# Kernel optimization log

Measured on AMD Instinct MI355X. Metric: run time of the kernel, lower is better.

Reference implementation:

```python
import jax, jax.numpy as jnp
import numpy as np

H = 16      # num_heads
G = 4       # num_groups (kv heads)
D = 128     # head_dim = embed_size // num_heads
E = 2048    # embed_size
FF = 8192   # GeGLU hidden = 4 * embed_size
EPS = 1e-6


def setup_inputs() -> dict:
    key = jax.random.key(0)
    ks = jax.random.split(key, 8)
    s = 0.02
    return {
        "x": jax.random.normal(ks[0], (2, 2048, E), dtype=jnp.float32),
        "wq": jax.random.normal(ks[1], (E, H * D), dtype=jnp.float32) * s,
        "wk": jax.random.normal(ks[2], (E, G * D), dtype=jnp.float32) * s,
        "wv": jax.random.normal(ks[3], (E, G * D), dtype=jnp.float32) * s,
        "wo": jax.random.normal(ks[4], (H * D, E), dtype=jnp.float32) * s,
        "norm1_w": jnp.ones((E,), dtype=jnp.float32),
        "norm2_w": jnp.ones((E,), dtype=jnp.float32),
        "w_in": jax.random.normal(ks[5], (E, 2 * FF), dtype=jnp.float32) * s,
        "w_out": jax.random.normal(ks[6], (FF, E), dtype=jnp.float32) * s,
    }


def rotate_half(t):
    t1, t2 = jnp.split(t, 2, axis=-1)
    return jnp.concatenate([-t2, t1], axis=-1)


def rope_cos_sin(n, d, dtype):
    inv_freq = 1.0 / (10000.0 ** (jnp.arange(0, d, 2, dtype=jnp.float32) / d))
    freqs = jnp.outer(jnp.arange(n, dtype=jnp.float32), inv_freq)  # [n, d/2]
    emb = jnp.concatenate([freqs, freqs], axis=-1)                 # [n, d]
    return jnp.cos(emb).astype(dtype), jnp.sin(emb).astype(dtype)


def rmsnorm(t, w):
    return t * jax.lax.rsqrt(jnp.mean(t * t, axis=-1, keepdims=True) + EPS) * w


def reference(x, wq, wk, wv, wo, norm1_w, norm2_w, w_in, w_out):
    b, n, _ = x.shape
    # q = k = v = x.view(b,n,H,D).transpose(1,2); RoPE applied to q,k (v stays raw)
    qh = x.reshape(b, n, H, D).transpose(0, 2, 1, 3)  # [b,H,n,D]
    cos, sin = rope_cos_sin(n, D, x.dtype)
    q_rot = qh * cos + rotate_half(qh) * sin          # q == k pre-RoPE -> same rotation
    k_rot = q_rot
    # flatten back: [b,n,E]; v flattened equals original x (unrotated)
    qf = q_rot.transpose(0, 2, 1, 3).reshape(b, n, E)
    kf = k_rot.transpose(0, 2, 1, 3).reshape(b, n, E)
    vf = x
    # GroupedQueryAttention: q->H heads, k/v->G kv-heads, causal
    qp = (qf @ wq).reshape(b, n, H, D).transpose(0, 2, 1, 3)          # [b,H,n,D]
    kp = (kf @ wk).reshape(b, n, G, D).transpose(0, 2, 1, 3)          # [b,G,n,D]
    vp = (vf @ wv).reshape(b, n, G, D).transpose(0, 2, 1, 3)          # [b,G,n,D]
    rep = H // G
    kp = jnp.repeat(kp, rep, axis=1)                                  # [b,H,n,D]
    vp = jnp.repeat(vp, rep, axis=1)
    scale = 1.0 / jnp.sqrt(jnp.asarray(D, dtype=x.dtype))
    scores = jnp.einsum("bhqd,bhkd->bhqk", qp, kp) * scale
    causal = jnp.tril(jnp.ones((n, n), dtype=bool))
    scores = jnp.where(causal, scores, jnp.asarray(-1e30, dtype=scores.dtype))
    attn = jax.nn.softmax(scores, axis=-1)
    ctx = jnp.einsum("bhqk,bhkd->bhqd", attn, vp)
    attn_out = ctx.transpose(0, 2, 1, 3).reshape(b, n, E) @ wo
    # residual + RMSNorm, GeGLU MLP, residual + RMSNorm
    h = rmsnorm(x + attn_out, norm1_w)
    hg = h @ w_in
    a, g = jnp.split(hg, 2, axis=-1)
    fc = (jax.nn.gelu(a, approximate=False) * g) @ w_out
    out = rmsnorm(h + fc, norm2_w)
    return out
```

## Files before the change

kernel.cpp:

```cpp
#include <hip/hip_runtime.h>
#include <hip/hip_bf16.h>

typedef __bf16 bf16x8 __attribute__((ext_vector_type(8)));
typedef short  s16x8  __attribute__((ext_vector_type(8)));
typedef float  f32x4  __attribute__((ext_vector_type(4)));

__device__ __forceinline__ float bf2f(short u) {
    unsigned x = ((unsigned)(unsigned short)u) << 16;
    float f; __builtin_memcpy(&f, &x, 4); return f;
}
__device__ __forceinline__ short f2bf(float f) {
    unsigned u; __builtin_memcpy(&u, &f, 4);
    unsigned r = (u + 0x7fff + ((u >> 16) & 1)) >> 16;
    return (short)r;
}
__device__ __forceinline__ bool src_is_f32(const void* ones_w) {
    return ((const unsigned short*)ones_w)[0] == 0;
}
__device__ __forceinline__ void gl2lds16(const short* g, short* lds_base) {
    __builtin_amdgcn_global_load_lds((const __attribute__((address_space(1))) void*)g,
                                     (__attribute__((address_space(3))) void*)lds_base, 16, 0, 0);
}
__device__ __forceinline__ bf16x8 lds_read_b128(const short* p) {
    bf16x8 r;
    asm volatile("ds_read_b128 %0, %1"
                 : "=v"(r)
                 : "v"((const __attribute__((address_space(3))) short*)p));
    return r;
}

__global__ __launch_bounds__(256) void rope_kernel(const void* __restrict__ xv, short* __restrict__ qf,
                                                   short* __restrict__ xbf, const void* __restrict__ n1w) {
    bool f32 = src_is_f32(n1w);
    int idx = blockIdx.x * 256 + threadIdx.x;
    int i    = idx & 63;
    int head = (idx >> 6) & 15;
    int t    = idx >> 10;
    int pos  = t & 2047;
    float inv = __expf(-9.210340371976184f * (float)i * (1.0f / 64.0f));
    float fr = (float)pos * inv;
    float s, c; sincosf(fr, &s, &c);
    long base = (long)t * 2048 + head * 128 + i;
    float v1, v2;
    if (f32) { v1 = ((const float*)xv)[base]; v2 = ((const float*)xv)[base + 64]; }
    else     { v1 = bf2f(((const short*)xv)[base]); v2 = bf2f(((const short*)xv)[base + 64]); }
    qf[base]      = f2bf(v1 * c - v2 * s);
    qf[base + 64] = f2bf(v2 * c + v1 * s);
    xbf[base]      = f2bf(v1);
    xbf[base + 64] = f2bf(v2);
}

__global__ __launch_bounds__(256) void transpose_any(const void* __restrict__ src, long soff, long soffz,
                                                     short* __restrict__ dst, long doffz,
                                                     int R, int C, int ld, const void* __restrict__ n1w, int force_bf16) {
    bool f32 = force_bf16 ? false : src_is_f32(n1w);
    __shared__ short tile[32][33];
    int tx = threadIdx.x & 31, ty = threadIdx.x >> 5;
    int c0 = blockIdx.x * 32, r0 = blockIdx.y * 32;
    long sz = soff + soffz * blockIdx.z;
    dst += doffz * blockIdx.z;
    #pragma unroll
    for (int i = 0; i < 32; i += 8) {
        long p = sz + (long)(r0 + ty + i) * ld + c0 + tx;
        tile[ty + i][tx] = f32 ? f2bf(((const float*)src)[p]) : ((const short*)src)[p];
    }
    __syncthreads();
    #pragma unroll
    for (int i = 0; i < 32; i += 8) dst[(long)(c0 + ty + i) * R + r0 + tx] = tile[tx][ty + i];
}

__global__ __launch_bounds__(256) void gemm_nt_kv(const short* __restrict__ A0, const short* __restrict__ A1, int lda,
                                                  const short* __restrict__ Bt0, const short* __restrict__ Bt1,
                                                  short* __restrict__ C0, short* __restrict__ C1, int ldc,
                                                  int M, int N, int K) {
    const short* A  = blockIdx.z ? A1 : A0;
    const short* Bt = blockIdx.z ? Bt1 : Bt0;
    short* C        = blockIdx.z ? C1 : C0;
    __shared__ short As[128 * 64];
    __shared__ short Bs[128 * 64];
    int tid = threadIdx.x;
    int w = tid >> 6, lane = tid & 63, quad = lane >> 4, l15 = lane & 15;
    int m0 = blockIdx.y * 128, n0 = blockIdx.x * 128;
    int wr = (w >> 1) * 64, wc = (w & 1) * 64;
    int srow = (lane >> 3), scol = (lane & 7) * 8;
    f32x4 acc[4][4] = {};
    for (int k0 = 0; k0 < K; k0 += 64) {
        __syncthreads();
        #pragma unroll
        for (int c = 0; c < 4; ++c) {
            int chunk = w * 4 + c;
            int row = chunk * 8 + srow;
            gl2lds16(&A [(long)(m0 + row) * lda + k0 + scol], As + chunk * 512);
            gl2lds16(&Bt[(long)(n0 + row) * K   + k0 + scol], Bs + chunk * 512);
        }
        __syncthreads();
        #pragma unroll
        for (int kk = 0; kk < 64; kk += 32) {
            bf16x8 a[4], b[4];
            #pragma unroll
            for (int i = 0; i < 4; ++i) a[i] = *(const bf16x8*)&As[(wr + 16 * i + l15) * 64 + kk + quad * 8];
            #pragma unroll
            for (int j = 0; j < 4; ++j) b[j] = *(const bf16x8*)&Bs[(wc + 16 * j + l15) * 64 + kk + quad * 8];
            #pragma unroll
            for (int i = 0; i < 4; ++i)
                #pragma unroll
                for (int j = 0; j < 4; ++j)
                    acc[i][j] = __builtin_amdgcn_mfma_f32_16x16x32_bf16(a[i], b[j], acc[i][j], 0, 0, 0);
        }
    }
    #pragma unroll
    for (int i = 0; i < 4; ++i)
        #pragma unroll
        for (int j = 0; j < 4; ++j)
            #pragma unroll
            for (int r = 0; r < 4; ++r)
                C[(long)(m0 + wr + 16 * i + quad * 4 + r) * ldc + n0 + wc + 16 * j + l15] = f2bf(acc[i][j][r]);
}

template<int GEGLU, int ACCUM>
__global__ __launch_bounds__(512) void gemm256(const short* __restrict__ A, int lda,
                                               const short* __restrict__ Bt, const short* __restrict__ Bt2, int ldb,
                                               short* __restrict__ C, short* __restrict__ C2, int ldc,
                                               int M, int N, int K) {
    __shared__ short As[2][256 * 64];
    __shared__ short Bs[2][256 * 64];
    int z = blockIdx.z;
    if (z) { Bt = Bt2; C = C2; }
    A += (long)z * K;
    int tid = threadIdx.x;
    int w = tid >> 6, lane = tid & 63, quad = lane >> 4, l15 = lane & 15;
    int sw = l15 & 7;
    int nbx = gridDim.x, nwg = nbx * gridDim.y;
    int bid = blockIdx.y * nbx + blockIdx.x;
    int swz = (bid & 7) * (nwg >> 3) + (bid >> 3);
    int n0 = (swz % nbx) * 256, m0 = (swz / nbx) * 256;
    int wr2 = (w >> 2) * 128;
    int wcb = (w & 3) * 64;
    int srow = lane >> 3;
    int scol = ((lane & 7) ^ srow) * 8;
    int NT = K >> 6;

    auto STAGE = [&](int bsel, int h, int tt) {
        long kk = (long)((tt < NT) ? tt : 0) * 64;
        int hb = (h & 1) * 8192;
        #pragma unroll
        for (int j = 0; j < 2; ++j) {
            int chunk = j * 8 + w;
            int row = (h & 1) * 128 + chunk * 8 + srow;
            if (h < 2) gl2lds16(&A [(long)(m0 + row) * lda + kk + scol], &As[bsel][hb + chunk * 512]);
            else       gl2lds16(&Bt[(long)(n0 + row) * ldb + kk + scol], &Bs[bsel][hb + chunk * 512]);
        }
    };

    f32x4 acc[8][4] = {};
    STAGE(0, 2, 0); STAGE(0, 3, 0); STAGE(0, 0, 0); STAGE(0, 1, 0);
    STAGE(1, 2, 1); STAGE(1, 3, 1);
    asm volatile("s_waitcnt vmcnt(4)");
    __builtin_amdgcn_s_barrier();

    for (int t = 0; t < NT; ++t) {
        int b = t & 1;
        const short* Ab = As[b];
        const short* Bb = Bs[b];
        bf16x8 bbf[4][2];
        #pragma unroll
        for (int q = 0; q < 4; ++q) {
            if (q == 0) {
                #pragma unroll
                for (int j = 0; j < 4; ++j) {
                    const short* rb = &Bb[(wcb + 16 * j + l15) * 64];
                    bbf[j][0] = lds_read_b128(rb + ((quad ^ sw) * 8));
                    bbf[j][1] = lds_read_b128(rb + (((4 + quad) ^ sw) * 8));
                }
            }
            const short* ra0 = &Ab[(wr2 + 32 * q + l15) * 64];
            const short* ra1 = ra0 + 16 * 64;
            bf16x8 a00 = lds_read_b128(ra0 + ((quad ^ sw) * 8));
            bf16x8 a01 = lds_read_b128(ra0 + (((4 + quad) ^ sw) * 8));
            bf16x8 a10 = lds_read_b128(ra1 + ((quad ^ sw) * 8));
            bf16x8 a11 = lds_read_b128(ra1 + (((4 + quad) ^ sw) * 8));
            if      (q == 0) STAGE(b ^ 1, 0, t + 1);
            else if (q == 1) STAGE(b ^ 1, 1, t + 1);
            else if (q == 2) STAGE(b,     2, t + 2);
            else { STAGE(b, 3, t + 2); asm volatile("s_waitcnt vmcnt(4)"); }
            asm volatile("s_waitcnt lgkmcnt(0)");
            __builtin_amdgcn_sched_barrier(0);
            __builtin_amdgcn_s_setprio(1);
            #pragma unroll
            for (int j = 0; j < 4; ++j) {
                acc[2*q  ][j] = __builtin_amdgcn_mfma_f32_16x16x32_bf16(a00, bbf[j][0], acc[2*q  ][j], 0, 0, 0);
                acc[2*q  ][j] = __builtin_amdgcn_mfma_f32_16x16x32_bf16(a01, bbf[j][1], acc[2*q  ][j], 0, 0, 0);
                acc[2*q+1][j] = __builtin_amdgcn_mfma_f32_16x16x32_bf16(a10, bbf[j][0], acc[2*q+1][j], 0, 0, 0);
                acc[2*q+1][j] = __builtin_amdgcn_mfma_f32_16x16x32_bf16(a11, bbf[j][1], acc[2*q+1][j], 0, 0, 0);
            }
            __builtin_amdgcn_s_setprio(0);
            __builtin_amdgcn_s_barrier();
        }
    }
    asm volatile("s_waitcnt vmcnt(0)");
    #pragma unroll
    for (int i = 0; i < 8; ++i)
        #pragma unroll
        for (int j = 0; j < 4; ++j)
            #pragma unroll
            for (int r = 0; r < 4; ++r) {
                long row = m0 + wr2 + 16 * i + quad * 4 + r;
                long col = n0 + wcb + 16 * j + l15;
                float v = acc[i][j][r];
                if (GEGLU) {
                    float av = bf2f(C[row * ldc + col]);
                    v = 0.5f * av * (1.0f + erff(av * 0.70710678118f)) * v;
                }
                if (ACCUM) v += bf2f(C[row * ldc + col]);
                C[row * ldc + col] = f2bf(v);
            }
}

__global__ __launch_bounds__(256) void attn_kernel(const short* __restrict__ qp, const short* __restrict__ qp2,
                                                   const short* __restrict__ kp,
                                                   const short* __restrict__ vpT, short* __restrict__ ctx) {
    __shared__ short Kt[64 * 128];
    __shared__ short Vt[128 * 64];
    __shared__ short plds[4][16 * 72];
    int bid = blockIdx.x;
    int qt = 31 - (bid >> 5);
    int b = (bid >> 4) & 1;
    int h = bid & 15;
    int tid = threadIdx.x;
    int w = tid >> 6, lane = tid & 63, quad = lane >> 4, l15 = lane & 15;
    int qs = qt * 64 + w * 16;
    int g = h >> 2;
    const float scale = 0.08838834764831845f;

    bf16x8 qa[4];
    {
        long qoff = (long)(b * 2048 + qs + l15) * 2048 + h * 128 + quad * 8;
        if (qp2) {
            #pragma unroll
            for (int c = 0; c < 4; ++c) {
                s16x8 u = *(const s16x8*)(qp  + qoff + 32 * c);
                s16x8 v = *(const s16x8*)(qp2 + qoff + 32 * c);
                s16x8 sres;
                #pragma unroll
                for (int k = 0; k < 8; ++k) sres[k] = f2bf(bf2f(u[k]) + bf2f(v[k]));
                qa[c] = *(bf16x8*)&sres;
            }
        } else {
            #pragma unroll
            for (int c = 0; c < 4; ++c) qa[c] = *(const bf16x8*)(qp + qoff + 32 * c);
        }
    }
    f32x4 o[8] = {};
    float mrow[4], lrow[4], alpha[4];
    #pragma unroll
    for (int r = 0; r < 4; ++r) { mrow[r] = -3e38f; lrow[r] = 0.f; }

    int krow = lane >> 4;
    int vrow = lane >> 3;
    int sw = l15 & 7;

    int kend = qt * 64 + 64;
    for (int k0 = 0; k0 < kend; k0 += 64) {
        __syncthreads();
        #pragma unroll
        for (int c = 0; c < 4; ++c) {
            int chunk = w * 4 + c;
            int kcol = ((lane & 15) ^ (((chunk & 1) << 2) + krow)) * 8;
            gl2lds16(&kp [(long)(b * 2048 + k0 + chunk * 4 + krow) * 512 + g * 128 + kcol], Kt + chunk * 512);
            int vcol = ((lane & 7) ^ vrow) * 8;
            gl2lds16(&vpT[(long)((b * 4 + g) * 128 + chunk * 8 + vrow) * 2048 + k0 + vcol], Vt + chunk * 512);
        }
        __syncthreads();
        f32x4 sc[4] = {};
        #pragma unroll
        for (int kt = 0; kt < 4; ++kt) {
            const short* kb = &Kt[(kt * 16 + l15) * 128];
            #pragma unroll
            for (int c = 0; c < 4; ++c)
                sc[kt] = __builtin_amdgcn_mfma_f32_16x16x32_bf16(qa[c],
                             *(const bf16x8*)(kb + (((quad + 4 * c) ^ sw) * 8)), sc[kt], 0, 0, 0);
        }
        float mx[4];
        #pragma unroll
        for (int r = 0; r < 4; ++r) mx[r] = -3e38f;
        #pragma unroll
        for (int kt = 0; kt < 4; ++kt)
            #pragma unroll
            for (int r = 0; r < 4; ++r) {
                int key = k0 + kt * 16 + l15;
                int q = qs + quad * 4 + r;
                float sv = sc[kt][r] * scale;
                if (key > q) sv = -1e30f;
                sc[kt][r] = sv;
                mx[r] = fmaxf(mx[r], sv);
            }
        #pragma unroll
        for (int r = 0; r < 4; ++r) {
            #pragma unroll
            for (int off = 8; off; off >>= 1) mx[r] = fmaxf(mx[r], __shfl_xor(mx[r], off, 64));
            float mn = fmaxf(mrow[r], mx[r]);
            alpha[r] = __expf(mrow[r] - mn);
            mrow[r] = mn;
        }
        float ls[4] = {0.f, 0.f, 0.f, 0.f};
        #pragma unroll
        for (int kt = 0; kt < 4; ++kt)
            #pragma unroll
            for (int r = 0; r < 4; ++r) {
                float pv = __expf(sc[kt][r] - mrow[r]);
                ls[r] += pv;
                plds[w][(quad * 4 + r) * 72 + kt * 16 + l15] = f2bf(pv);
            }
        #pragma unroll
        for (int r = 0; r < 4; ++r) {
            #pragma unroll
            for (int off = 8; off; off >>= 1) ls[r] += __shfl_xor(ls[r], off, 64);
            lrow[r] = lrow[r] * alpha[r] + ls[r];
        }
        #pragma unroll
        for (int dt = 0; dt < 8; ++dt)
            #pragma unroll
            for (int r = 0; r < 4; ++r) o[dt][r] *= alpha[r];
        bf16x8 pa0 = *(const bf16x8*)&plds[w][l15 * 72 + quad * 8];
        bf16x8 pa1 = *(const bf16x8*)&plds[w][l15 * 72 + 32 + quad * 8];
        #pragma unroll
        for (int dt = 0; dt < 8; ++dt) {
            const short* vb = &Vt[(dt * 16 + l15) * 64];
            o[dt] = __builtin_amdgcn_mfma_f32_16x16x32_bf16(pa0,
                        *(const bf16x8*)(vb + ((quad ^ sw) * 8)),        o[dt], 0, 0, 0);
            o[dt] = __builtin_amdgcn_mfma_f32_16x16x32_bf16(pa1,
                        *(const bf16x8*)(vb + (((quad + 4) ^ sw) * 8)),  o[dt], 0, 0, 0);
        }
    }
    #pragma unroll
    for (int dt = 0; dt < 8; ++dt)
        #pragma unroll
        for (int r = 0; r < 4; ++r) {
            int q = qs + quad * 4 + r;
            float inv_l = lrow[r] > 0.f ? 1.0f / lrow[r] : 0.f;
            ctx[(long)(b * 2048 + q) * 2048 + h * 128 + dt * 16 + l15] = f2bf(o[dt][r] * inv_l);
        }
}

template<int OUT_ADAPT>
__global__ __launch_bounds__(256) void rmsnorm_res(const short* __restrict__ a, const short* __restrict__ b,
                                                   const short* __restrict__ c,
                                                   const void* __restrict__ w, void* __restrict__ out) {
    bool f32 = src_is_f32(w);
    int t = blockIdx.x, tid = threadIdx.x;
    long base = (long)t * 2048 + tid * 8;
    s16x8 av = *(const s16x8*)(a + base);
    s16x8 bv = *(const s16x8*)(b + base);
    float v[8]; float ss = 0.f;
    #pragma unroll
    for (int k = 0; k < 8; ++k) v[k] = bf2f(av[k]) + bf2f(bv[k]);
    if (c) {
        s16x8 cv = *(const s16x8*)(c + base);
        #pragma unroll
        for (int k = 0; k < 8; ++k) v[k] += bf2f(cv[k]);
    }
    #pragma unroll
    for (int k = 0; k < 8; ++k) ss += v[k] * v[k];
    #pragma unroll
    for (int off = 32; off; off >>= 1) ss += __shfl_xor(ss, off, 64);
    __shared__ float red[4];
    if ((tid & 63) == 0) red[tid >> 6] = ss;
    __syncthreads();
    float tot = red[0] + red[1] + red[2] + red[3];
    float rs = rsqrtf(tot * (1.0f / 2048.0f) + 1e-6f);
    float wv[8];
    if (f32) {
        #pragma unroll
        for (int k = 0; k < 8; ++k) wv[k] = ((const float*)w)[tid * 8 + k];
    } else {
        s16x8 w8 = *(const s16x8*)((const short*)w + tid * 8);
        #pragma unroll
        for (int k = 0; k < 8; ++k) wv[k] = bf2f(w8[k]);
    }
    if (OUT_ADAPT && f32) {
        float* o = (float*)out;
        #pragma unroll
        for (int k = 0; k < 8; ++k) o[base + k] = v[k] * rs * wv[k];
    } else {
        short* o = (short*)out;
        s16x8 ov;
        #pragma unroll
        for (int k = 0; k < 8; ++k) ov[k] = f2bf(v[k] * rs * wv[k]);
        *(s16x8*)(o + base) = ov;
    }
}

extern "C" void kernel_launch(void* const* d_in, const int* in_sizes, int n_in,
                              void* d_out, int out_size, void* d_ws, size_t ws_size,
                              hipStream_t stream) {
    const void* x     = d_in[0];
    const void* wq    = d_in[1];
    const void* wk    = d_in[2];
    const void* wv    = d_in[3];
    const void* wo    = d_in[4];
    const void* n1w   = d_in[5];
    const void* n2w   = d_in[6];
    const void* w_in  = d_in[7];
    const void* w_out = d_in[8];
    char* ws = (char*)d_ws;
    short* WT  = (short*)(ws);
    short* WTv = (short*)(ws + (2ll  << 20));
    short* kp  = (short*)(ws + (16ll << 20));
    short* vp  = (short*)(ws + (20ll << 20));
    short* vpT = (short*)(ws + (24ll << 20));
    short* ctx = (short*)(ws + (28ll << 20));
    short* xbf = (short*)(ws + (44ll << 20));
    short* qf  = (short*)(ws + (60ll << 20));
    short* ao2 = qf;
    short* act = (short*)(ws + (16ll << 20));
    short* qp  = (short*)(ws + (80ll << 20));
    short* h   = (short*)(ws + (96ll << 20));
    short* ao = qp; short* fc = qp;
    bool big_ws = ws_size >= (144ll << 20);
    short* WT2 = (short*)(ws + (112ll << 20));
    short* qp2 = WT2;
    short* fc2 = (short*)(ws + (128ll << 20));

    rope_kernel<<<16384, 256, 0, stream>>>(x, qf, xbf, n1w);

    transpose_any<<<dim3(64, 64), 256, 0, stream>>>(wq, 0, 0, WT, 0, 2048, 2048, 2048, n1w, 0);
    if (big_ws)
        gemm256<0, 0><<<dim3(8, 16, 2), 512, 0, stream>>>(qf, 2048, WT, WT + 1024, 2048, qp, qp2, 2048, 4096, 2048, 1024);
    else
        gemm256<0, 0><<<dim3(8, 16), 512, 0, stream>>>(qf, 2048, WT, WT, 2048, qp, qp, 2048, 4096, 2048, 2048);

    transpose_any<<<dim3(16, 64), 256, 0, stream>>>(wk, 0, 0, WT,  0, 2048, 512, 512, n1w, 0);
    transpose_any<<<dim3(16, 64), 256, 0, stream>>>(wv, 0, 0, WTv, 0, 2048, 512, 512, n1w, 0);
    gemm_nt_kv<<<dim3(4, 32, 2), 256, 0, stream>>>(qf, xbf, 2048, WT, WTv, kp, vp, 512, 4096, 512, 2048);

    transpose_any<<<dim3(16, 64, 2), 256, 0, stream>>>(vp, 0, (long)2048 * 512, vpT, (long)512 * 2048,
                                                       2048, 512, 512, n1w, 1);

    attn_kernel<<<1024, 256, 0, stream>>>(qp, big_ws ? qp2 : (const short*)nullptr, kp, vpT, ctx);

    transpose_any<<<dim3(64, 64), 256, 0, stream>>>(wo, 0, 0, WT, 0, 2048, 2048, 2048, n1w, 0);
    gemm256<0, 0><<<dim3(8, 16, 2), 512, 0, stream>>>(ctx, 2048, WT, WT + 1024, 2048, ao, ao2, 2048, 4096, 2048, 1024);

    rmsnorm_res<0><<<4096, 256, 0, stream>>>(xbf, ao, ao2, n1w, h);

    for (int q = 0; q < 4; ++q) {
        transpose_any<<<dim3(128, 64), 256, 0, stream>>>(w_in, (long)q * 4096, 0, WT, 0, 2048, 4096, 16384, n1w, 0);
        if (q < 2)
            gemm256<0, 0><<<dim3(16, 16), 512, 0, stream>>>(h, 2048, WT, WT, 2048, act + q * 4096, act, 8192, 4096, 4096, 2048);
        else
            gemm256<1, 0><<<dim3(16, 16), 512, 0, stream>>>(h, 2048, WT, WT, 2048, act + (q - 2) * 4096, act, 8192, 4096, 4096, 2048);
    }

    if (big_ws) {
        transpose_any<<<dim3(64, 128, 2), 256, 0, stream>>>(w_out, 0, (long)4096 * 2048, WT, (112ll << 20) / 2,
                                                            4096, 2048, 2048, n1w, 0);
        gemm256<0, 0><<<dim3(8, 16, 2), 512, 0, stream>>>(act, 8192, WT, WT2, 4096, fc, fc2, 2048, 4096, 2048, 4096);
        rmsnorm_res<1><<<4096, 256, 0, stream>>>(h, fc, fc2, n2w, d_out);
    } else {
        transpose_any<<<dim3(64, 128), 256, 0, stream>>>(w_out, 0, 0, WT, 0, 4096, 2048, 2048, n1w, 0);
        gemm256<0, 0><<<dim3(8, 16), 512, 0, stream>>>(act, 8192, WT, WT, 4096, fc, fc, 2048, 4096, 2048, 4096);
        transpose_any<<<dim3(64, 128), 256, 0, stream>>>(w_out, (long)4096 * 2048, 0, WT, 0, 4096, 2048, 2048, n1w, 0);
        gemm256<0, 1><<<dim3(8, 16), 512, 0, stream>>>(act + 4096, 8192, WT, WT, 4096, fc, fc, 2048, 4096, 2048, 4096);
        rmsnorm_res<1><<<4096, 256, 0, stream>>>(h, fc, (const short*)nullptr, n2w, d_out);
    }
}
```

Baseline: 1.033 ms.

## Fuse Q and K projections, prefetch A fragments, batch GeGLU GEMM launches

The Q and K projections, which share the rotated input, now run as one wider gemm256 launch that writes columns past the Q width into the K buffer. This removes the split-K Q path and the per-element Q summation in the attention kernel. The V projection gets its own smaller launch. Inside gemm256, the second A fragment for the next sub-step is loaded from LDS while the current MFMAs issue, with partial lgkmcnt waits so LDS reads overlap compute. When the large workspace is available, the four GeGLU weight transposes and GEMMs are merged into two z-batched launches. The cost is more register pressure and more complex wait-count logic, and the fused QK grid of 10x16 tiles may balance unevenly across compute units.

Result: faster. 1.010 ms (-2.3%).

```diff
diff --git a/kernel.cpp b/kernel.cpp
--- a/kernel.cpp
+++ b/kernel.cpp
@@ -69,13 +69,8 @@
     for (int i = 0; i < 32; i += 8) dst[(long)(c0 + ty + i) * R + r0 + tx] = tile[tx][ty + i];
 }
 
-__global__ __launch_bounds__(256) void gemm_nt_kv(const short* __restrict__ A0, const short* __restrict__ A1, int lda,
-                                                  const short* __restrict__ Bt0, const short* __restrict__ Bt1,
-                                                  short* __restrict__ C0, short* __restrict__ C1, int ldc,
-                                                  int M, int N, int K) {
-    const short* A  = blockIdx.z ? A1 : A0;
-    const short* Bt = blockIdx.z ? Bt1 : Bt0;
-    short* C        = blockIdx.z ? C1 : C0;
+__global__ __launch_bounds__(256) void gemm_nt(const short* __restrict__ A, int lda, const short* __restrict__ Bt,
+                                               short* __restrict__ C, int ldc, int M, int N, int K) {
     __shared__ short As[128 * 64];
     __shared__ short Bs[128 * 64];
     int tid = threadIdx.x;
@@ -121,12 +116,13 @@
 __global__ __launch_bounds__(512) void gemm256(const short* __restrict__ A, int lda,
                                                const short* __restrict__ Bt, const short* __restrict__ Bt2, int ldb,
                                                short* __restrict__ C, short* __restrict__ C2, int ldc,
-                                               int M, int N, int K) {
+                                               int M, int N, int K, int zAoff,
+                                               short* __restrict__ Ck, int qn, int ldck) {
     __shared__ short As[2][256 * 64];
     __shared__ short Bs[2][256 * 64];
     int z = blockIdx.z;
     if (z) { Bt = Bt2; C = C2; }
-    A += (long)z * K;
+    A += (long)z * zAoff;
     int tid = threadIdx.x;
     int w = tid >> 6, lane = tid & 63, quad = lane >> 4, l15 = lane & 15;
     int sw = l15 & 7;
@@ -163,8 +159,10 @@
         const short* Ab = As[b];
         const short* Bb = Bs[b];
         bf16x8 bbf[4][2];
+        bf16x8 aP0, aP1;
         #pragma unroll
         for (int q = 0; q < 4; ++q) {
+            const short* ra = &Ab[(wr2 + 32 * q + l15) * 64];
             if (q == 0) {
                 #pragma unroll
                 for (int j = 0; j < 4; ++j) {
@@ -172,32 +170,46 @@
                     bbf[j][0] = lds_read_b128(rb + ((quad ^ sw) * 8));
                     bbf[j][1] = lds_read_b128(rb + (((4 + quad) ^ sw) * 8));
                 }
-            }
-            const short* ra0 = &Ab[(wr2 + 32 * q + l15) * 64];
-            const short* ra1 = ra0 + 16 * 64;
-            bf16x8 a00 = lds_read_b128(ra0 + ((quad ^ sw) * 8));
-            bf16x8 a01 = lds_read_b128(ra0 + (((4 + quad) ^ sw) * 8));
-            bf16x8 a10 = lds_read_b128(ra1 + ((quad ^ sw) * 8));
-            bf16x8 a11 = lds_read_b128(ra1 + (((4 + quad) ^ sw) * 8));
+                aP0 = lds_read_b128(ra + ((quad ^ sw) * 8));
+                aP1 = lds_read_b128(ra + (((4 + quad) ^ sw) * 8));
+            }
+            bf16x8 a10 = lds_read_b128(ra + 16 * 64 + ((quad ^ sw) * 8));
+            bf16x8 a11 = lds_read_b128(ra + 16 * 64 + (((4 + quad) ^ sw) * 8));
             if      (q == 0) STAGE(b ^ 1, 0, t + 1);
             else if (q == 1) STAGE(b ^ 1, 1, t + 1);
             else if (q == 2) STAGE(b,     2, t + 2);
             else { STAGE(b, 3, t + 2); asm volatile("s_waitcnt vmcnt(4)"); }
-            asm volatile("s_waitcnt lgkmcnt(0)");
+            asm volatile("s_waitcnt lgkmcnt(2)");
             __builtin_amdgcn_sched_barrier(0);
             __builtin_amdgcn_s_setprio(1);
             #pragma unroll
             for (int j = 0; j < 4; ++j) {
-                acc[2*q  ][j] = __builtin_amdgcn_mfma_f32_16x16x32_bf16(a00, bbf[j][0], acc[2*q  ][j], 0, 0, 0);
-                acc[2*q  ][j] = __builtin_amdgcn_mfma_f32_16x16x32_bf16(a01, bbf[j][1], acc[2*q  ][j], 0, 0, 0);
+                acc[2*q  ][j] = __builtin_amdgcn_mfma_f32_16x16x32_bf16(aP0, bbf[j][0], acc[2*q  ][j], 0, 0, 0);
+                acc[2*q  ][j] = __builtin_amdgcn_mfma_f32_16x16x32_bf16(aP1, bbf[j][1], acc[2*q  ][j], 0, 0, 0);
+            }
+            bf16x8 nP0, nP1;
+            if (q < 3) {
+                const short* rn = ra + 32 * 64;
+                nP0 = lds_read_b128(rn + ((quad ^ sw) * 8));
+                nP1 = lds_read_b128(rn + (((4 + quad) ^ sw) * 8));
+            }
+            __builtin_amdgcn_sched_barrier(0);
+            if (q < 3) asm volatile("s_waitcnt lgkmcnt(2)");
+            else       asm volatile("s_waitcnt lgkmcnt(0)");
+            __builtin_amdgcn_sched_barrier(0);
+            #pragma unroll
+            for (int j = 0; j < 4; ++j) {
                 acc[2*q+1][j] = __builtin_amdgcn_mfma_f32_16x16x32_bf16(a10, bbf[j][0], acc[2*q+1][j], 0, 0, 0);
                 acc[2*q+1][j] = __builtin_amdgcn_mfma_f32_16x16x32_bf16(a11, bbf[j][1], acc[2*q+1][j], 0, 0, 0);
             }
             __builtin_amdgcn_s_setprio(0);
             __builtin_amdgcn_s_barrier();
+            if (q < 3) { aP0 = nP0; aP1 = nP1; }
         }
     }
     asm volatile("s_waitcnt vmcnt(0)");
+    int ncoff = 0;
+    if (n0 >= qn) { C = Ck; ldc = ldck; ncoff = qn; }
     #pragma unroll
     for (int i = 0; i < 8; ++i)
         #pragma unroll
@@ -205,7 +217,7 @@
             #pragma unroll
             for (int r = 0; r < 4; ++r) {
                 long row = m0 + wr2 + 16 * i + quad * 4 + r;
-                long col = n0 + wcb + 16 * j + l15;
+                long col = n0 + wcb + 16 * j + l15 - ncoff;
                 float v = acc[i][j][r];
                 if (GEGLU) {
                     float av = bf2f(C[row * ldc + col]);
@@ -216,8 +228,7 @@
             }
 }
 
-__global__ __launch_bounds__(256) void attn_kernel(const short* __restrict__ qp, const short* __restrict__ qp2,
-                                                   const short* __restrict__ kp,
+__global__ __launch_bounds__(256) void attn_kernel(const short* __restrict__ qp, const short* __restrict__ kp,
                                                    const short* __restrict__ vpT, short* __restrict__ ctx) {
     __shared__ short Kt[64 * 128];
     __shared__ short Vt[128 * 64];
@@ -234,21 +245,9 @@
 
     bf16x8 qa[4];
     {
-        long qoff = (long)(b * 2048 + qs + l15) * 2048 + h * 128 + quad * 8;
-        if (qp2) {
-            #pragma unroll
-            for (int c = 0; c < 4; ++c) {
-                s16x8 u = *(const s16x8*)(qp  + qoff + 32 * c);
-                s16x8 v = *(const s16x8*)(qp2 + qoff + 32 * c);
-                s16x8 sres;
-                #pragma unroll
-                for (int k = 0; k < 8; ++k) sres[k] = f2bf(bf2f(u[k]) + bf2f(v[k]));
-                qa[c] = *(bf16x8*)&sres;
-            }
-        } else {
-            #pragma unroll
-            for (int c = 0; c < 4; ++c) qa[c] = *(const bf16x8*)(qp + qoff + 32 * c);
-        }
+        const short* qbase = qp + (long)(b * 2048 + qs + l15) * 2048 + h * 128 + quad * 8;
+        #pragma unroll
+        for (int c = 0; c < 4; ++c) qa[c] = *(const bf16x8*)(qbase + 32 * c);
     }
     f32x4 o[8] = {};
     float mrow[4], lrow[4], alpha[4];
@@ -403,8 +402,8 @@
     const void* w_in  = d_in[7];
     const void* w_out = d_in[8];
     char* ws = (char*)d_ws;
+    const int QBIG = 1 << 30;
     short* WT  = (short*)(ws);
-    short* WTv = (short*)(ws + (2ll  << 20));
     short* kp  = (short*)(ws + (16ll << 20));
     short* vp  = (short*)(ws + (20ll << 20));
     short* vpT = (short*)(ws + (24ll << 20));
@@ -418,49 +417,62 @@
     short* ao = qp; short* fc = qp;
     bool big_ws = ws_size >= (144ll << 20);
     short* WT2 = (short*)(ws + (112ll << 20));
-    short* qp2 = WT2;
     short* fc2 = (short*)(ws + (128ll << 20));
 
     rope_kernel<<<16384, 256, 0, stream>>>(x, qf, xbf, n1w);
 
     transpose_any<<<dim3(64, 64), 256, 0, stream>>>(wq, 0, 0, WT, 0, 2048, 2048, 2048, n1w, 0);
-    if (big_ws)
-        gemm256<0, 0><<<dim3(8, 16, 2), 512, 0, stream>>>(qf, 2048, WT, WT + 1024, 2048, qp, qp2, 2048, 4096, 2048, 1024);
-    else
-        gemm256<0, 0><<<dim3(8, 16), 512, 0, stream>>>(qf, 2048, WT, WT, 2048, qp, qp, 2048, 4096, 2048, 2048);
-
-    transpose_any<<<dim3(16, 64), 256, 0, stream>>>(wk, 0, 0, WT,  0, 2048, 512, 512, n1w, 0);
-    transpose_any<<<dim3(16, 64), 256, 0, stream>>>(wv, 0, 0, WTv, 0, 2048, 512, 512, n1w, 0);
-    gemm_nt_kv<<<dim3(4, 32, 2), 256, 0, stream>>>(qf, xbf, 2048, WT, WTv, kp, vp, 512, 4096, 512, 2048);
+    transpose_any<<<dim3(16, 64), 256, 0, stream>>>(wk, 0, 0, WT + (long)2048 * 2048, 0, 2048, 512, 512, n1w, 0);
+    gemm256<0, 0><<<dim3(10, 16), 512, 0, stream>>>(qf, 2048, WT, WT, 2048, qp, qp, 2048,
+                                                    4096, 2560, 2048, 0, kp, 2048, 512);
+
+    transpose_any<<<dim3(16, 64), 256, 0, stream>>>(wv, 0, 0, WT, 0, 2048, 512, 512, n1w, 0);
+    gemm_nt<<<dim3(4, 32), 256, 0, stream>>>(xbf, 2048, WT, vp, 512, 4096, 512, 2048);
 
     transpose_any<<<dim3(16, 64, 2), 256, 0, stream>>>(vp, 0, (long)2048 * 512, vpT, (long)512 * 2048,
                                                        2048, 512, 512, n1w, 1);
 
-    attn_kernel<<<1024, 256, 0, stream>>>(qp, big_ws ? qp2 : (const short*)nullptr, kp, vpT, ctx);
+    attn_kernel<<<1024, 256, 0, stream>>>(qp, kp, vpT, ctx);
 
     transpose_any<<<dim3(64, 64), 256, 0, stream>>>(wo, 0, 0, WT, 0, 2048, 2048, 2048, n1w, 0);
-    gemm256<0, 0><<<dim3(8, 16, 2), 512, 0, stream>>>(ctx, 2048, WT, WT + 1024, 2048, ao, ao2, 2048, 4096, 2048, 1024);
+    gemm256<0, 0><<<dim3(8, 16, 2), 512, 0, stream>>>(ctx, 2048, WT, WT + 1024, 2048, ao, ao2, 2048,
+                                                      4096, 2048, 1024, 1024, (short*)nullptr, QBIG, 0);
 
     rmsnorm_res<0><<<4096, 256, 0, stream>>>(xbf, ao, ao2, n1w, h);
 
-    for (int q = 0; q < 4; ++q) {
-        transpose_any<<<dim3(128, 64), 256, 0, stream>>>(w_in, (long)q * 4096, 0, WT, 0, 2048, 4096, 16384, n1w, 0);
-        if (q < 2)
-            gemm256<0, 0><<<dim3(16, 16), 512, 0, stream>>>(h, 2048, WT, WT, 2048, act + q * 4096, act, 8192, 4096, 4096, 2048);
-        else
-            gemm256<1, 0><<<dim3(16, 16), 512, 0, stream>>>(h, 2048, WT, WT, 2048, act + (q - 2) * 4096, act, 8192, 4096, 4096, 2048);
-    }
-
     if (big_ws) {
-        transpose_any<<<dim3(64, 128, 2), 256, 0, stream>>>(w_out, 0, (long)4096 * 2048, WT, (112ll << 20) / 2,
+        long dz = (long)(WT2 - WT);
+        transpose_any<<<dim3(128, 64, 2), 256, 0, stream>>>(w_in, 0, 4096, WT, dz, 2048, 4096, 16384, n1w, 0);
+        gemm256<0, 0><<<dim3(16, 16, 2), 512, 0, stream>>>(h, 2048, WT, WT2, 2048, act, act + 4096, 8192,
+                                                           4096, 4096, 2048, 0, (short*)nullptr, QBIG, 0);
+        transpose_any<<<dim3(128, 64, 2), 256, 0, stream>>>(w_in, (long)2 * 4096, 4096, WT, dz, 2048, 4096, 16384, n1w, 0);
+        gemm256<1, 0><<<dim3(16, 16, 2), 512, 0, stream>>>(h, 2048, WT, WT2, 2048, act, act + 4096, 8192,
+                                                           4096, 4096, 2048, 0, (short*)nullptr, QBIG, 0);
+    } else {
+        for (int q = 0; q < 4; ++q) {
+            transpose_any<<<dim3(128, 64), 256, 0, stream>>>(w_in, (long)q * 4096, 0, WT, 0, 2048, 4096, 16384, n1w, 0);
+            if (q < 2)
+                gemm256<0, 0><<<dim3(16, 16), 512, 0, stream>>>(h, 2048, WT, WT, 2048, act + q * 4096, act, 8192,
+                                                                4096, 4096, 2048, 0, (short*)nullptr, QBIG, 0);
+            else
+                gemm256<1, 0><<<dim3(16, 16), 512, 0, stream>>>(h, 2048, WT, WT, 2048, act + (q - 2) * 4096, act, 8192,
+                                                                4096, 4096, 2048, 0, (short*)nullptr, QBIG, 0);
+        }
+    }
+
+    if (big_ws) {
+        transpose_any<<<dim3(64, 128, 2), 256, 0, stream>>>(w_out, 0, (long)4096 * 2048, WT, (long)(WT2 - WT),
                                                             4096, 2048, 2048, n1w, 0);
-        gemm256<0, 0><<<dim3(8, 16, 2), 512, 0, stream>>>(act, 8192, WT, WT2, 4096, fc, fc2, 2048, 4096, 2048, 4096);
+        gemm256<0, 0><<<dim3(8, 16, 2), 512, 0, stream>>>(act, 8192, WT, WT2, 4096, fc, fc2, 2048,
+                                                          4096, 2048, 4096, 4096, (short*)nullptr, QBIG, 0);
         rmsnorm_res<1><<<4096, 256, 0, stream>>>(h, fc, fc2, n2w, d_out);
     } else {
         transpose_any<<<dim3(64, 128), 256, 0, stream>>>(w_out, 0, 0, WT, 0, 4096, 2048, 2048, n1w, 0);
-        gemm256<0, 0><<<dim3(8, 16), 512, 0, stream>>>(act, 8192, WT, WT, 4096, fc, fc, 2048, 4096, 2048, 4096);
+        gemm256<0, 0><<<dim3(8, 16), 512, 0, stream>>>(act, 8192, WT, WT, 4096, fc, fc, 2048,
+                                                       4096, 2048, 4096, 0, (short*)nullptr, QBIG, 0);
         transpose_any<<<dim3(64, 128), 256, 0, stream>>>(w_out, (long)4096 * 2048, 0, WT, 0, 4096, 2048, 2048, n1w, 0);
-        gemm256<0, 1><<<dim3(8, 16), 512, 0, stream>>>(act + 4096, 8192, WT, WT, 4096, fc, fc, 2048, 4096, 2048, 4096);
+        gemm256<0, 1><<<dim3(8, 16), 512, 0, stream>>>(act + 4096, 8192, WT, WT, 4096, fc, fc, 2048,
+                                                       4096, 2048, 4096, 0, (short*)nullptr, QBIG, 0);
         rmsnorm_res<1><<<4096, 256, 0, stream>>>(h, fc, (const short*)nullptr, n2w, d_out);
     }
 }
```
